# Optimization experiments

Hardware: AMD Instinct MI355X
Metric: run time of the kernel (lower is better)

Reference implementation:

```python
import jax, jax.numpy as jnp
import numpy as np


def window_partition(x, w):
    # x: [B,H,W,C] -> [B*(H/w)*(W/w), w, w, C]
    B, H, W, C = x.shape
    x = x.reshape(B, H // w, w, W // w, w, C)
    return jnp.transpose(x, (0, 1, 3, 2, 4, 5)).reshape(-1, w, w, C)


def window_reverse(xw, w, H, W):
    B = xw.shape[0] // ((H // w) * (W // w))
    x = xw.reshape(B, H // w, W // w, w, w, -1)
    return jnp.transpose(x, (0, 1, 3, 2, 4, 5)).reshape(B, H, W, -1)


def chess_partition(x, w):
    # x: [B,H,W,C] -> [B*w*w, H/w, W/w, C] (strided / chessboard grouping)
    B, H, W, C = x.shape
    x = x.reshape(B, H // w, w, W // w, w, C)
    return jnp.transpose(x, (0, 2, 4, 1, 3, 5)).reshape(-1, H // w, W // w, C)


def chess_reverse(xw, w, H, W):
    B = xw.shape[0] // (w * w)
    x = xw.reshape(B, w, w, H // w, W // w, -1)
    return jnp.transpose(x, (0, 3, 1, 4, 2, 5)).reshape(B, H, W, -1)


def _attn_block(x, wq, bq, wk, bk, wv, bv, gamma, win, part, rev):
    # x: [B,C,H,W]; 1x1-conv QKV inside partitioned windows, bmm softmax attention
    B, C, H, W = x.shape
    xw = part(jnp.transpose(x, (0, 2, 3, 1)), win)      # [B_, h, w, C]
    B_, h, w, _ = xw.shape
    xw = jnp.transpose(xw, (0, 3, 1, 2))                # [B_, C, h, w]
    q = (jnp.einsum('oc,bchw->bhwo', wq, xw) + bq).reshape(B_, h * w, -1)   # [B_,N,C/4]
    k = (jnp.einsum('oc,bchw->bohw', wk, xw) + bk[:, None, None]).reshape(B_, -1, h * w)  # [B_,C/4,N]
    v = (jnp.einsum('oc,bchw->bohw', wv, xw) + bv[:, None, None]).reshape(B_, C, h * w)   # [B_,C,N]
    attn = jax.nn.softmax(jnp.einsum('bnc,bcm->bnm', q, k), axis=-1)        # [B_,N,N]
    out = jnp.einsum('bcm,bnm->bnc', v, attn).reshape(B_, h, w, C)
    out = jnp.transpose(rev(out, win, H, W), (0, 3, 1, 2))                  # [B,C,H,W]
    return gamma * out + x


def setup_inputs() -> dict:
    key = jax.random.key(0)
    ks = jax.random.split(key, 16)
    B, C, H, W = 8, 64, 192, 192
    Cq = C // 4
    s = 0.05
    inp = {'x': jax.random.normal(ks[0], (B, C, H, W), jnp.float32)}
    names = ['wq1', 'bq1', 'wk1', 'bk1', 'wv1', 'bv1',
             'wq2', 'bq2', 'wk2', 'bk2', 'wv2', 'bv2']
    shapes = [(Cq, C), (Cq,), (Cq, C), (Cq,), (C, C), (C,),
              (Cq, C), (Cq,), (Cq, C), (Cq,), (C, C), (C,)]
    for i, (n, sh) in enumerate(zip(names, shapes)):
        inp[n] = jax.random.normal(ks[i + 1], sh, jnp.float32) * s
    # gamma is zero-init in torch; use small random so attention path contributes
    inp['gamma1'] = jax.random.normal(ks[13], (1,), jnp.float32) * 0.5
    inp['gamma2'] = jax.random.normal(ks[14], (1,), jnp.float32) * 0.5
    return inp


def reference(x, wq1, bq1, wk1, bk1, wv1, bv1, gamma1,
              wq2, bq2, wk2, bk2, wv2, bv2, gamma2):
    out1 = _attn_block(x, wq1, bq1, wk1, bk1, wv1, bv1, gamma1,
                       4, window_partition, window_reverse)
    out = _attn_block(out1, wq2, bq2, wk2, bk2, wv2, bv2, gamma2,
                      8, chess_partition, chess_reverse)
    return out
```

## Files before the change

### kernel.cpp

```cpp
#include <hip/hip_runtime.h>
#include <hip/hip_bf16.h>

#define HW 36864

typedef __attribute__((ext_vector_type(8))) short short8;
typedef __attribute__((ext_vector_type(16))) float f32x16;

__device__ __forceinline__ float BLO(unsigned u) { return __uint_as_float(u << 16); }
__device__ __forceinline__ float BHI(unsigned u) { return __uint_as_float(u & 0xffff0000u); }
__device__ __forceinline__ unsigned short f2bf(float f) {
    unsigned u = __float_as_uint(f);
    u += 0x7fffu + ((u >> 16) & 1u);
    return (unsigned short)(u >> 16);
}
__device__ __forceinline__ unsigned pk2(float lo, float hi) {
    unsigned r;
    asm("v_cvt_pk_bf16_f32 %0, %1, %2" : "=v"(r) : "v"(lo), "v"(hi));
    return r;
}
__device__ __forceinline__ void plswap(unsigned &a, unsigned &b) {
    asm volatile("v_permlane32_swap_b32 %0, %1" : "+v"(a), "+v"(b));
}

union FragW { unsigned u[4]; short8 s; };


__global__ __launch_bounds__(256) void to_nhwc_kernel(
    const float* __restrict__ x, char* __restrict__ xh)
{
    __shared__ unsigned lds[32 * 193];
    const int bid = blockIdx.x;
    const int b = bid / 192, y = bid % 192;
    const int tid = threadIdx.x;
    const int cp = tid >> 3, xq8 = tid & 7;

    const float4* rA = (const float4*)(x + ((size_t)b * 64 + 2 * cp) * HW + (size_t)y * 192);
    const float4* rB = (const float4*)(x + ((size_t)b * 64 + 2 * cp + 1) * HW + (size_t)y * 192);
    #pragma unroll
    for (int i = 0; i < 6; ++i) {
        const int f = 8 * i + xq8;
        const float4 a = rA[f];
        const float4 c = rB[f];
        const int px = f * 4;
        lds[cp * 193 + px + 0] = pk2(a.x, c.x);
        lds[cp * 193 + px + 1] = pk2(a.y, c.y);
        lds[cp * 193 + px + 2] = pk2(a.z, c.z);
        lds[cp * 193 + px + 3] = pk2(a.w, c.w);
    }
    __syncthreads();

    char* dst = xh + ((size_t)b * HW + (size_t)y * 192) * 128;
    #pragma unroll
    for (int j = 0; j < 6; ++j) {
        const int idx = j * 256 + tid;
        const int px = idx >> 3, q = idx & 7;
        uint4 v;
        v.x = lds[(4 * q + 0) * 193 + px];
        v.y = lds[(4 * q + 1) * 193 + px];
        v.z = lds[(4 * q + 2) * 193 + px];
        v.w = lds[(4 * q + 3) * 193 + px];
        *(uint4*)(dst + px * 128 + q * 16) = v;
    }
}

__global__ __launch_bounds__(256) void attn1n_kernel(
    char* __restrict__ xh,
    const float* __restrict__ wq, const float* __restrict__ bq,
    const float* __restrict__ wk, const float* __restrict__ bk,
    const float* __restrict__ wv, const float* __restrict__ bv,
    const float* __restrict__ gamma)
{
    __shared__ char smem[4 * 8192];

    const int tid   = threadIdx.x;
    const int wv_id = tid >> 6;
    const int lane  = tid & 63;
    const int l32   = lane & 31;
    const int h     = lane >> 5;
    char* VsW = smem + wv_id * 8192;

    const int gw0 = blockIdx.x * 16 + wv_id * 4;

    f32x16 zf;
    #pragma unroll
    for (int r = 0; r < 16; ++r) zf[r] = 0.f;

    FragW wqkf[4], wvf[2][4];
    {
        const float4* wrow4 = (const float4*)((l32 < 16) ? (wq + l32 * 64)
                                                         : (wk + (l32 - 16) * 64));
        #pragma unroll
        for (int cc = 0; cc < 4; ++cc) {
            const float4 a = wrow4[cc * 4 + 2 * h];
            const float4 b = wrow4[cc * 4 + 2 * h + 1];
            wqkf[cc].u[0] = pk2(a.x, a.y); wqkf[cc].u[1] = pk2(a.z, a.w);
            wqkf[cc].u[2] = pk2(b.x, b.y); wqkf[cc].u[3] = pk2(b.z, b.w);
        }
        #pragma unroll
        for (int ot = 0; ot < 2; ++ot) {
            const float4* wvr4 = (const float4*)(wv + (size_t)(ot * 32 + l32) * 64);
            #pragma unroll
            for (int cc = 0; cc < 4; ++cc) {
                const float4 a = wvr4[cc * 4 + 2 * h];
                const float4 b = wvr4[cc * 4 + 2 * h + 1];
                wvf[ot][cc].u[0] = pk2(a.x, a.y); wvf[ot][cc].u[1] = pk2(a.z, a.w);
                wvf[ot][cc].u[2] = pk2(b.x, b.y); wvf[ot][cc].u[3] = pk2(b.z, b.w);
            }
        }
    }
    float bqv[8], bkv[8], bvv[2][16];
    #pragma unroll
    for (int r = 0; r < 8; ++r) {
        const int c = (r & 3) + 8 * (r >> 2) + 4 * h;
        bqv[r] = bq[c];
        bkv[r] = bk[c];
    }
    #pragma unroll
    for (int ot = 0; ot < 2; ++ot)
        #pragma unroll
        for (int r = 0; r < 16; ++r)
            bvv[ot][r] = bv[ot * 32 + (r & 3) + 8 * (r >> 2) + 4 * h];

    FragW Ilo, Ihi;
    #pragma unroll
    for (int j = 0; j < 4; ++j) {
        const int k0 = 8 * h + 2 * j;
        unsigned lo  = (l32 == k0)      ? 0x3F80u : 0u;
        unsigned hi  = (l32 == k0 + 1)  ? 0x3F80u : 0u;
        Ilo.u[j] = lo | (hi << 16);
        unsigned lo2 = (l32 == 16 + k0)     ? 0x3F80u : 0u;
        unsigned hi2 = (l32 == 16 + k0 + 1) ? 0x3F80u : 0u;
        Ihi.u[j] = lo2 | (hi2 << 16);
    }

    size_t px1[2];
    #pragma unroll
    for (int t = 0; t < 2; ++t) {
        const int gwin = gw0 + 2 * t + (l32 >> 4);
        const int b = gwin / 2304;
        const int rem = gwin % 2304;
        const int Y = rem / 48, X = rem % 48;
        const int yy = Y * 4 + ((l32 >> 2) & 3);
        const int xx = X * 4 + (l32 & 3);
        px1[t] = ((size_t)b * HW + (size_t)yy * 192 + xx) * 128;
    }

    FragW qf[2], kf[2];
    #pragma unroll
    for (int t = 0; t < 2; ++t) {
        const char* rec = xh + px1[t];
        FragW xw[4];
        #pragma unroll
        for (int cc = 0; cc < 4; ++cc)
            xw[cc].s = *(const short8*)(rec + cc * 32 + 16 * h);

        f32x16 dqk = zf;
        #pragma unroll
        for (int cc = 0; cc < 4; ++cc)
            dqk = __builtin_amdgcn_mfma_f32_32x32x16_bf16(wqkf[cc].s, xw[cc].s, dqk, 0, 0, 0);

        {
            float q0[8];
            #pragma unroll
            for (int r = 0; r < 8; ++r) q0[r] = dqk[r] + bqv[r];
            unsigned A0 = pk2(q0[0], q0[1]), B0 = pk2(q0[2], q0[3]);
            unsigned C0 = pk2(q0[4], q0[5]), D0 = pk2(q0[6], q0[7]);
            plswap(A0, C0); plswap(B0, D0);
            qf[t].u[0] = A0; qf[t].u[1] = B0; qf[t].u[2] = C0; qf[t].u[3] = D0;
        }
        {
            float k0[8];
            #pragma unroll
            for (int r = 0; r < 8; ++r) k0[r] = dqk[8 + r] + bkv[r];
            unsigned A0 = pk2(k0[0], k0[1]), B0 = pk2(k0[2], k0[3]);
            unsigned C0 = pk2(k0[4], k0[5]), D0 = pk2(k0[6], k0[7]);
            plswap(A0, C0); plswap(B0, D0);
            kf[t].u[0] = A0; kf[t].u[1] = B0; kf[t].u[2] = C0; kf[t].u[3] = D0;
        }

        #pragma unroll
        for (int ot = 0; ot < 2; ++ot) {
            f32x16 dv = zf;
            #pragma unroll
            for (int cc = 0; cc < 4; ++cc)
                dv = __builtin_amdgcn_mfma_f32_32x32x16_bf16(wvf[ot][cc].s, xw[cc].s, dv, 0, 0, 0);
            #pragma unroll
            for (int r = 0; r < 16; ++r) {
                const int ch = ot * 32 + (r & 3) + 8 * (r >> 2) + 4 * h;
                *(unsigned short*)(VsW + ((ch * 128 + 2 * (t * 32 + l32)) ^ ((ch & 7) << 4)))
                    = f2bf(dv[r] + bvv[ot][r]);
            }
        }
    }
    __syncthreads();

    const float g = gamma[0];
    const bool wa = (l32 < 16);

    #pragma unroll
    for (int t = 0; t < 2; ++t) {
        f32x16 sT = __builtin_amdgcn_mfma_f32_32x32x16_bf16(kf[t].s, qf[t].s, zf, 0, 0, 0);

        float e[8];
        #pragma unroll
        for (int j = 0; j < 8; ++j) e[j] = __expf(wa ? sT[j] : sT[8 + j]);
        float ls = ((e[0] + e[1]) + (e[2] + e[3])) + ((e[4] + e[5]) + (e[6] + e[7]));
        ls += __shfl_xor(ls, 32);

        unsigned A0 = pk2(e[0], e[1]), B0 = pk2(e[2], e[3]);
        unsigned C0 = pk2(e[4], e[5]), D0 = pk2(e[6], e[7]);
        plswap(A0, C0); plswap(B0, D0);
        FragW pa, pb;
        pa.u[0] = wa ? A0 : 0u; pa.u[1] = wa ? B0 : 0u;
        pa.u[2] = wa ? C0 : 0u; pa.u[3] = wa ? D0 : 0u;
        pb.u[0] = wa ? 0u : A0; pb.u[1] = wa ? 0u : B0;
        pb.u[2] = wa ? 0u : C0; pb.u[3] = wa ? 0u : D0;

        f32x16 acc0 = zf, acc1 = zf;
        #pragma unroll
        for (int wsx = 0; wsx < 2; ++wsx) {
            const short8 pfrag = wsx ? pb.s : pa.s;
            const int mbase = t * 64 + wsx * 32 + 16 * h;
            const int ch0 = l32, ch1 = 32 + l32;
            const short8 v0 = *(const short8*)(VsW + ((ch0 * 128 + mbase) ^ ((ch0 & 7) << 4)));
            const short8 v1 = *(const short8*)(VsW + ((ch1 * 128 + mbase) ^ ((ch1 & 7) << 4)));
            acc0 = __builtin_amdgcn_mfma_f32_32x32x16_bf16(v0, pfrag, acc0, 0, 0, 0);
            acc1 = __builtin_amdgcn_mfma_f32_32x32x16_bf16(v1, pfrag, acc1, 0, 0, 0);
        }

        const float inv = 1.f / ls;

        char* rec = xh + px1[t];
        FragW x0, x1, x2, x3;
        x0.s = *(const short8*)(rec + 0 * 32 + 16 * h);
        x1.s = *(const short8*)(rec + 1 * 32 + 16 * h);
        x2.s = *(const short8*)(rec + 2 * 32 + 16 * h);
        x3.s = *(const short8*)(rec + 3 * 32 + 16 * h);
        f32x16 r01 = __builtin_amdgcn_mfma_f32_32x32x16_bf16(Ihi.s, x1.s, zf, 0, 0, 0);
        r01 = __builtin_amdgcn_mfma_f32_32x32x16_bf16(Ilo.s, x0.s, r01, 0, 0, 0);
        f32x16 r23 = __builtin_amdgcn_mfma_f32_32x32x16_bf16(Ihi.s, x3.s, zf, 0, 0, 0);
        r23 = __builtin_amdgcn_mfma_f32_32x32x16_bf16(Ilo.s, x2.s, r23, 0, 0, 0);

        #pragma unroll
        for (int q = 0; q < 4; ++q) {
            const float a0 = fmaf(g, acc0[4*q+0] * inv, r01[4*q+0]);
            const float a1 = fmaf(g, acc0[4*q+1] * inv, r01[4*q+1]);
            const float a2 = fmaf(g, acc0[4*q+2] * inv, r01[4*q+2]);
            const float a3 = fmaf(g, acc0[4*q+3] * inv, r01[4*q+3]);
            uint2 wA; wA.x = pk2(a0, a1); wA.y = pk2(a2, a3);
            *(uint2*)(rec + 16 * q + 8 * h) = wA;
            const float b0 = fmaf(g, acc1[4*q+0] * inv, r23[4*q+0]);
            const float b1 = fmaf(g, acc1[4*q+1] * inv, r23[4*q+1]);
            const float b2 = fmaf(g, acc1[4*q+2] * inv, r23[4*q+2]);
            const float b3 = fmaf(g, acc1[4*q+3] * inv, r23[4*q+3]);
            uint2 wB; wB.x = pk2(b0, b1); wB.y = pk2(b2, b3);
            *(uint2*)(rec + 64 + 16 * q + 8 * h) = wB;
        }
    }
}

#define KT_OFF 0
#define VS_OFF 18432

__global__ __launch_bounds__(576) void attn2n_kernel(
    char* __restrict__ xh,
    const float* __restrict__ wq, const float* __restrict__ bq,
    const float* __restrict__ wk, const float* __restrict__ bk,
    const float* __restrict__ wv, const float* __restrict__ bv,
    const float* __restrict__ gamma)
{
    __shared__ char smem[92160];

    const int wid = blockIdx.x;
    const int b  = wid >> 6;
    const int a  = wid & 7;
    const int c0 = (wid >> 3) & 7;

    const int tid = threadIdx.x;
    const int wv_id = tid >> 6;
    const int l32 = tid & 31;
    const int h   = (tid >> 5) & 1;
    const int n0  = wv_id * 64;

    f32x16 zf;
    #pragma unroll
    for (int r = 0; r < 16; ++r) zf[r] = 0.f;

    FragW wqkf[4], wvf[2][4];
    {
        const float4* wrow4 = (const float4*)((l32 < 16) ? (wq + l32 * 64)
                                                         : (wk + (l32 - 16) * 64));
        #pragma unroll
        for (int cc = 0; cc < 4; ++cc) {
            const float4 a4 = wrow4[cc * 4 + 2 * h];
            const float4 b4 = wrow4[cc * 4 + 2 * h + 1];
            wqkf[cc].u[0] = pk2(a4.x, a4.y); wqkf[cc].u[1] = pk2(a4.z, a4.w);
            wqkf[cc].u[2] = pk2(b4.x, b4.y); wqkf[cc].u[3] = pk2(b4.z, b4.w);
        }
        #pragma unroll
        for (int ot = 0; ot < 2; ++ot) {
            const float4* wvr4 = (const float4*)(wv + (size_t)(ot * 32 + l32) * 64);
            #pragma unroll
            for (int cc = 0; cc < 4; ++cc) {
                const float4 a4 = wvr4[cc * 4 + 2 * h];
                const float4 b4 = wvr4[cc * 4 + 2 * h + 1];
                wvf[ot][cc].u[0] = pk2(a4.x, a4.y); wvf[ot][cc].u[1] = pk2(a4.z, a4.w);
                wvf[ot][cc].u[2] = pk2(b4.x, b4.y); wvf[ot][cc].u[3] = pk2(b4.z, b4.w);
            }
        }
    }
    float bias_qk[16], bvv[2][16];
    #pragma unroll
    for (int r = 0; r < 8; ++r) {
        const int c = (r & 3) + 8 * (r >> 2) + 4 * h;
        bias_qk[r] = bq[c];
        bias_qk[8 + r] = bk[c];
    }
    #pragma unroll
    for (int ot = 0; ot < 2; ++ot)
        #pragma unroll
        for (int r = 0; r < 16; ++r)
            bvv[ot][r] = bv[ot * 32 + (r & 3) + 8 * (r >> 2) + 4 * h];

    FragW Ilo, Ihi;
    #pragma unroll
    for (int j = 0; j < 4; ++j) {
        const int k0 = 8 * h + 2 * j;
        unsigned lo  = (l32 == k0)      ? 0x3F80u : 0u;
        unsigned hi  = (l32 == k0 + 1)  ? 0x3F80u : 0u;
        Ilo.u[j] = lo | (hi << 16);
        unsigned lo2 = (l32 == 16 + k0)     ? 0x3F80u : 0u;
        unsigned hi2 = (l32 == 16 + k0 + 1) ? 0x3F80u : 0u;
        Ihi.u[j] = lo2 | (hi2 << 16);
    }

    size_t prec[2];
    FragW qfr[2];
    #pragma unroll
    for (int t = 0; t < 2; ++t) {
        const int m = n0 + t * 32 + l32;
        const int i = m / 24, j = m - i * 24;
        prec[t] = ((size_t)b * HW + (size_t)(a + 8 * i) * 192 + (c0 + 8 * j)) * 128;
        const char* rec = xh + prec[t];

        FragW xw[4];
        #pragma unroll
        for (int cc = 0; cc < 4; ++cc)
            xw[cc].s = *(const short8*)(rec + cc * 32 + 16 * h);

        f32x16 dqk = zf;
        #pragma unroll
        for (int cc = 0; cc < 4; ++cc)
            dqk = __builtin_amdgcn_mfma_f32_32x32x16_bf16(wqkf[cc].s, xw[cc].s, dqk, 0, 0, 0);

        {
            float q0[8];
            #pragma unroll
            for (int r = 0; r < 8; ++r) q0[r] = dqk[r] + bias_qk[r];
            unsigned A0 = pk2(q0[0], q0[1]), B0 = pk2(q0[2], q0[3]);
            unsigned C0 = pk2(q0[4], q0[5]), D0 = pk2(q0[6], q0[7]);
            plswap(A0, C0); plswap(B0, D0);
            qfr[t].u[0] = A0; qfr[t].u[1] = B0; qfr[t].u[2] = C0; qfr[t].u[3] = D0;
        }
        #pragma unroll
        for (int r = 8; r < 16; ++r) {
            const int c = (r & 3) + 8 * ((r >> 2) & 1) + 4 * h;
            *(unsigned short*)(smem + KT_OFF + ((m * 32 + 2 * c) ^ (((m >> 2) & 3) << 4)))
                = f2bf(dqk[r] + bias_qk[r]);
        }
        #pragma unroll
        for (int ot = 0; ot < 2; ++ot) {
            f32x16 dv = zf;
            #pragma unroll
            for (int cc = 0; cc < 4; ++cc)
                dv = __builtin_amdgcn_mfma_f32_32x32x16_bf16(wvf[ot][cc].s, xw[cc].s, dv, 0, 0, 0);
            #pragma unroll
            for (int r = 0; r < 16; ++r) {
                const int ch = ot * 32 + (r & 3) + 8 * (r >> 2) + 4 * h;
                *(unsigned short*)(smem + VS_OFF + ((ch * 1152 + 2 * m) ^ ((ch & 7) << 4)))
                    = f2bf(dv[r] + bvv[ot][r]);
            }
        }
    }
    __syncthreads();

    const short8 qf0 = qfr[0].s, qf1 = qfr[1].s;
    f32x16 accA = zf, accB = zf, accC = zf, accD = zf;
    float ls0 = 0.f, ls1 = 0.f;
    const int chA = l32, chB = 32 + l32;
    const int swzA = (chA & 7) << 4, swzB = (chB & 7) << 4;

    #pragma unroll 1
    for (int mt = 0; mt < 18; ++mt) {
        const int m0 = mt * 32;
        const int mr = m0 + l32;
        const short8 kf = *(const short8*)(smem + KT_OFF + ((mr * 32 + 16 * h) ^ (((mr >> 2) & 3) << 4)));
        f32x16 s0 = __builtin_amdgcn_mfma_f32_32x32x16_bf16(kf, qf0, zf, 0, 0, 0);
        f32x16 s1 = __builtin_amdgcn_mfma_f32_32x32x16_bf16(kf, qf1, zf, 0, 0, 0);

        const short8 vA0 = *(const short8*)(smem + VS_OFF + ((chA * 1152 + 2 * (m0 + 8 * h)) ^ swzA));
        const short8 vA1 = *(const short8*)(smem + VS_OFF + ((chA * 1152 + 2 * (m0 + 16 + 8 * h)) ^ swzA));
        const short8 vB0 = *(const short8*)(smem + VS_OFF + ((chB * 1152 + 2 * (m0 + 8 * h)) ^ swzB));
        const short8 vB1 = *(const short8*)(smem + VS_OFF + ((chB * 1152 + 2 * (m0 + 16 + 8 * h)) ^ swzB));

        #pragma unroll
        for (int r = 0; r < 16; ++r) s0[r] = __expf(s0[r]);
        #pragma unroll
        for (int r = 0; r < 16; ++r) s1[r] = __expf(s1[r]);
        ls0 += ((s0[0]+s0[1])+(s0[2]+s0[3])) + ((s0[4]+s0[5])+(s0[6]+s0[7]))
             + ((s0[8]+s0[9])+(s0[10]+s0[11])) + ((s0[12]+s0[13])+(s0[14]+s0[15]));
        ls1 += ((s1[0]+s1[1])+(s1[2]+s1[3])) + ((s1[4]+s1[5])+(s1[6]+s1[7]))
             + ((s1[8]+s1[9])+(s1[10]+s1[11])) + ((s1[12]+s1[13])+(s1[14]+s1[15]));

        FragW pf00, pf01, pf10, pf11;
        {
            unsigned A0 = pk2(s0[0], s0[1]), B0 = pk2(s0[2], s0[3]);
            unsigned C0 = pk2(s0[4], s0[5]), D0 = pk2(s0[6], s0[7]);
            plswap(A0, C0); plswap(B0, D0);
            pf00.u[0] = A0; pf00.u[1] = B0; pf00.u[2] = C0; pf00.u[3] = D0;
            unsigned E0 = pk2(s0[8], s0[9]),  F0 = pk2(s0[10], s0[11]);
            unsigned G0 = pk2(s0[12], s0[13]), H0 = pk2(s0[14], s0[15]);
            plswap(E0, G0); plswap(F0, H0);
            pf01.u[0] = E0; pf01.u[1] = F0; pf01.u[2] = G0; pf01.u[3] = H0;
            unsigned A1 = pk2(s1[0], s1[1]), B1 = pk2(s1[2], s1[3]);
            unsigned C1 = pk2(s1[4], s1[5]), D1 = pk2(s1[6], s1[7]);
            plswap(A1, C1); plswap(B1, D1);
            pf10.u[0] = A1; pf10.u[1] = B1; pf10.u[2] = C1; pf10.u[3] = D1;
            unsigned E1 = pk2(s1[8], s1[9]),  F1 = pk2(s1[10], s1[11]);
            unsigned G1 = pk2(s1[12], s1[13]), H1 = pk2(s1[14], s1[15]);
            plswap(E1, G1); plswap(F1, H1);
            pf11.u[0] = E1; pf11.u[1] = F1; pf11.u[2] = G1; pf11.u[3] = H1;
        }

        accA = __builtin_amdgcn_mfma_f32_32x32x16_bf16(vA0, pf00.s, accA, 0, 0, 0);
        accA = __builtin_amdgcn_mfma_f32_32x32x16_bf16(vA1, pf01.s, accA, 0, 0, 0);
        accB = __builtin_amdgcn_mfma_f32_32x32x16_bf16(vB0, pf00.s, accB, 0, 0, 0);
        accB = __builtin_amdgcn_mfma_f32_32x32x16_bf16(vB1, pf01.s, accB, 0, 0, 0);
        accC = __builtin_amdgcn_mfma_f32_32x32x16_bf16(vA0, pf10.s, accC, 0, 0, 0);
        accC = __builtin_amdgcn_mfma_f32_32x32x16_bf16(vA1, pf11.s, accC, 0, 0, 0);
        accD = __builtin_amdgcn_mfma_f32_32x32x16_bf16(vB0, pf10.s, accD, 0, 0, 0);
        accD = __builtin_amdgcn_mfma_f32_32x32x16_bf16(vB1, pf11.s, accD, 0, 0, 0);
    }

    ls0 += __shfl_xor(ls0, 32);
    ls1 += __shfl_xor(ls1, 32);
    const float g2 = gamma[0];
    const float inv0 = 1.f / ls0, inv1 = 1.f / ls1;

    #pragma unroll
    for (int t = 0; t < 2; ++t) {
        char* rec = xh + prec[t];
        FragW x0, x1, x2, x3;
        x0.s = *(const short8*)(rec + 0 * 32 + 16 * h);
        x1.s = *(const short8*)(rec + 1 * 32 + 16 * h);
        x2.s = *(const short8*)(rec + 2 * 32 + 16 * h);
        x3.s = *(const short8*)(rec + 3 * 32 + 16 * h);
        f32x16 r01 = __builtin_amdgcn_mfma_f32_32x32x16_bf16(Ihi.s, x1.s, zf, 0, 0, 0);
        r01 = __builtin_amdgcn_mfma_f32_32x32x16_bf16(Ilo.s, x0.s, r01, 0, 0, 0);
        f32x16 r23 = __builtin_amdgcn_mfma_f32_32x32x16_bf16(Ihi.s, x3.s, zf, 0, 0, 0);
        r23 = __builtin_amdgcn_mfma_f32_32x32x16_bf16(Ilo.s, x2.s, r23, 0, 0, 0);

        const f32x16 aclo = t ? accC : accA;
        const f32x16 achi = t ? accD : accB;
        const float inv = t ? inv1 : inv0;

        #pragma unroll
        for (int q = 0; q < 4; ++q) {
            const float a0 = fmaf(g2, aclo[4*q+0] * inv, r01[4*q+0]);
            const float a1 = fmaf(g2, aclo[4*q+1] * inv, r01[4*q+1]);
            const float a2 = fmaf(g2, aclo[4*q+2] * inv, r01[4*q+2]);
            const float a3 = fmaf(g2, aclo[4*q+3] * inv, r01[4*q+3]);
            uint2 wA; wA.x = pk2(a0, a1); wA.y = pk2(a2, a3);
            *(uint2*)(rec + 16 * q + 8 * h) = wA;
            const float b0 = fmaf(g2, achi[4*q+0] * inv, r23[4*q+0]);
            const float b1 = fmaf(g2, achi[4*q+1] * inv, r23[4*q+1]);
            const float b2 = fmaf(g2, achi[4*q+2] * inv, r23[4*q+2]);
            const float b3 = fmaf(g2, achi[4*q+3] * inv, r23[4*q+3]);
            uint2 wB; wB.x = pk2(b0, b1); wB.y = pk2(b2, b3);
            *(uint2*)(rec + 64 + 16 * q + 8 * h) = wB;
        }
    }
}

__global__ __launch_bounds__(256) void to_nchw_kernel(
    float* __restrict__ out, const char* __restrict__ xh)
{
    __shared__ char smem[24576];

    const int bid = blockIdx.x;
    const int b = bid / 192, y = bid % 192;
    const int tid = threadIdx.x;

    const char* src = xh + ((size_t)b * HW + (size_t)y * 192) * 128;
    #pragma unroll
    for (int k = 0; k < 6; ++k) {
        const int off = k * 4096 + tid * 16;
        const int xq = off >> 7;
        const int gq = (off >> 4) & 7;
        const short8 v = *(const short8*)(src + off);
        *(short8*)(smem + (xq << 7) + (((gq ^ (xq & 7)) << 4))) = v;
    }
    __syncthreads();

    const int w = tid >> 6, lane = tid & 63;
    const size_t rowbase = (size_t)b * 64 * HW + (size_t)y * 192;

    #pragma unroll
    for (int it = 0; it < 24; ++it) {
        const int tt = it * 4 + w;
        const int chp = tt & 31;
        const int xb = tt >> 5;
        const int xx = xb * 64 + lane;
        const int byte_in_rec = chp * 4;
        const int gq = byte_in_rec >> 4;
        const unsigned v = *(const unsigned*)(smem + (xx << 7)
                            + ((gq ^ (xx & 7)) << 4) + (byte_in_rec & 15));
        const size_t o0 = rowbase + (size_t)(2 * chp) * HW + xx;
        out[o0]      = BLO(v);
        out[o0 + HW] = BHI(v);
    }
}

extern "C" void kernel_launch(void* const* d_in, const int* in_sizes, int n_in,
                              void* d_out, int out_size, void* d_ws, size_t ws_size,
                              hipStream_t stream)
{
    const float* x   = (const float*)d_in[0];
    const float* wq1 = (const float*)d_in[1];
    const float* bq1 = (const float*)d_in[2];
    const float* wk1 = (const float*)d_in[3];
    const float* bk1 = (const float*)d_in[4];
    const float* wv1 = (const float*)d_in[5];
    const float* bv1 = (const float*)d_in[6];
    const float* wq2 = (const float*)d_in[7];
    const float* bq2 = (const float*)d_in[8];
    const float* wk2 = (const float*)d_in[9];
    const float* bk2 = (const float*)d_in[10];
    const float* wv2 = (const float*)d_in[11];
    const float* bv2 = (const float*)d_in[12];
    const float* g1  = (const float*)d_in[13];
    const float* g2  = (const float*)d_in[14];
    float* out = (float*)d_out;
    char* xh = (char*)d_ws;

    to_nhwc_kernel<<<dim3(1536), dim3(256), 0, stream>>>(x, xh);

    attn1n_kernel<<<dim3(1152), dim3(256), 0, stream>>>(
        xh, wq1, bq1, wk1, bk1, wv1, bv1, g1);

    attn2n_kernel<<<dim3(512), dim3(576), 0, stream>>>(
        xh, wq2, bq2, wk2, bk2, wv2, bv2, g2);

    to_nchw_kernel<<<dim3(1536), dim3(256), 0, stream>>>(out, xh);
}
```

Baseline: 149.9 us.

## Use exp2 with log2e-scaled Q, prefetch K, compute row sums via MFMA

Folds log2(e) into Q when it is produced, so the softmax can call exp2f instead of __expf. The chess-block loop now prefetches the next K fragment from LDS one iteration ahead. It also replaces the scalar VALU row-sum reductions and the cross-lane shuffle with MFMAs against an all-ones bf16 matrix. This moves adds from the VALU to the matrix core, but it adds four MFMAs per iteration, more accumulator registers, and sums bf16-rounded probabilities, which costs some precision.

Measured after the change: 172.6 us. +15.1%, slower.

```diff
diff --git a/kernel.cpp b/kernel.cpp
--- a/kernel.cpp
+++ b/kernel.cpp
@@ -2,6 +2,7 @@
 #include <hip/hip_bf16.h>
 
 #define HW 36864
+#define LOG2E 1.44269504088896f
 
 typedef __attribute__((ext_vector_type(8))) short short8;
 typedef __attribute__((ext_vector_type(16))) float f32x16;
@@ -162,7 +163,7 @@
         {
             float q0[8];
             #pragma unroll
-            for (int r = 0; r < 8; ++r) q0[r] = dqk[r] + bqv[r];
+            for (int r = 0; r < 8; ++r) q0[r] = (dqk[r] + bqv[r]) * LOG2E;
             unsigned A0 = pk2(q0[0], q0[1]), B0 = pk2(q0[2], q0[3]);
             unsigned C0 = pk2(q0[4], q0[5]), D0 = pk2(q0[6], q0[7]);
             plswap(A0, C0); plswap(B0, D0);
@@ -203,7 +204,7 @@
 
         float e[8];
         #pragma unroll
-        for (int j = 0; j < 8; ++j) e[j] = __expf(wa ? sT[j] : sT[8 + j]);
+        for (int j = 0; j < 8; ++j) e[j] = exp2f(wa ? sT[j] : sT[8 + j]);
         float ls = ((e[0] + e[1]) + (e[2] + e[3])) + ((e[4] + e[5]) + (e[6] + e[7]));
         ls += __shfl_xor(ls, 32);
 
@@ -333,6 +334,8 @@
         unsigned hi2 = (l32 == 16 + k0 + 1) ? 0x3F80u : 0u;
         Ihi.u[j] = lo2 | (hi2 << 16);
     }
+    FragW ones;
+    ones.u[0] = ones.u[1] = ones.u[2] = ones.u[3] = 0x3F803F80u;
 
     size_t prec[2];
     FragW qfr[2];
@@ -356,7 +359,7 @@
         {
             float q0[8];
             #pragma unroll
-            for (int r = 0; r < 8; ++r) q0[r] = dqk[r] + bias_qk[r];
+            for (int r = 0; r < 8; ++r) q0[r] = (dqk[r] + bias_qk[r]) * LOG2E;
             unsigned A0 = pk2(q0[0], q0[1]), B0 = pk2(q0[2], q0[3]);
             unsigned C0 = pk2(q0[4], q0[5]), D0 = pk2(q0[6], q0[7]);
             plswap(A0, C0); plswap(B0, D0);
@@ -386,17 +389,24 @@
 
     const short8 qf0 = qfr[0].s, qf1 = qfr[1].s;
     f32x16 accA = zf, accB = zf, accC = zf, accD = zf;
-    float ls0 = 0.f, ls1 = 0.f;
+    f32x16 accS0 = zf, accS1 = zf;
     const int chA = l32, chB = 32 + l32;
     const int swzA = (chA & 7) << 4, swzB = (chB & 7) << 4;
+
+    short8 kfc = *(const short8*)(smem + KT_OFF + ((l32 * 32 + 16 * h) ^ (((l32 >> 2) & 3) << 4)));
 
     #pragma unroll 1
     for (int mt = 0; mt < 18; ++mt) {
         const int m0 = mt * 32;
-        const int mr = m0 + l32;
-        const short8 kf = *(const short8*)(smem + KT_OFF + ((mr * 32 + 16 * h) ^ (((mr >> 2) & 3) << 4)));
-        f32x16 s0 = __builtin_amdgcn_mfma_f32_32x32x16_bf16(kf, qf0, zf, 0, 0, 0);
-        f32x16 s1 = __builtin_amdgcn_mfma_f32_32x32x16_bf16(kf, qf1, zf, 0, 0, 0);
+
+        short8 kfn = kfc;
+        if (mt < 17) {
+            const int mr = m0 + 32 + l32;
+            kfn = *(const short8*)(smem + KT_OFF + ((mr * 32 + 16 * h) ^ (((mr >> 2) & 3) << 4)));
+        }
+
+        f32x16 s0 = __builtin_amdgcn_mfma_f32_32x32x16_bf16(kfc, qf0, zf, 0, 0, 0);
+        f32x16 s1 = __builtin_amdgcn_mfma_f32_32x32x16_bf16(kfc, qf1, zf, 0, 0, 0);
 
         const short8 vA0 = *(const short8*)(smem + VS_OFF + ((chA * 1152 + 2 * (m0 + 8 * h)) ^ swzA));
         const short8 vA1 = *(const short8*)(smem + VS_OFF + ((chA * 1152 + 2 * (m0 + 16 + 8 * h)) ^ swzA));
@@ -404,13 +414,9 @@
         const short8 vB1 = *(const short8*)(smem + VS_OFF + ((chB * 1152 + 2 * (m0 + 16 + 8 * h)) ^ swzB));
 
         #pragma unroll
-        for (int r = 0; r < 16; ++r) s0[r] = __expf(s0[r]);
-        #pragma unroll
-        for (int r = 0; r < 16; ++r) s1[r] = __expf(s1[r]);
-        ls0 += ((s0[0]+s0[1])+(s0[2]+s0[3])) + ((s0[4]+s0[5])+(s0[6]+s0[7]))
-             + ((s0[8]+s0[9])+(s0[10]+s0[11])) + ((s0[12]+s0[13])+(s0[14]+s0[15]));
-        ls1 += ((s1[0]+s1[1])+(s1[2]+s1[3])) + ((s1[4]+s1[5])+(s1[6]+s1[7]))
-             + ((s1[8]+s1[9])+(s1[10]+s1[11])) + ((s1[12]+s1[13])+(s1[14]+s1[15]));
+        for (int r = 0; r < 16; ++r) s0[r] = exp2f(s0[r]);
+        #pragma unroll
+        for (int r = 0; r < 16; ++r) s1[r] = exp2f(s1[r]);
 
         FragW pf00, pf01, pf10, pf11;
         {
@@ -440,12 +446,17 @@
         accC = __builtin_amdgcn_mfma_f32_32x32x16_bf16(vA1, pf11.s, accC, 0, 0, 0);
         accD = __builtin_amdgcn_mfma_f32_32x32x16_bf16(vB0, pf10.s, accD, 0, 0, 0);
         accD = __builtin_amdgcn_mfma_f32_32x32x16_bf16(vB1, pf11.s, accD, 0, 0, 0);
-    }
-
-    ls0 += __shfl_xor(ls0, 32);
-    ls1 += __shfl_xor(ls1, 32);
+
+        accS0 = __builtin_amdgcn_mfma_f32_32x32x16_bf16(ones.s, pf00.s, accS0, 0, 0, 0);
+        accS0 = __builtin_amdgcn_mfma_f32_32x32x16_bf16(ones.s, pf01.s, accS0, 0, 0, 0);
+        accS1 = __builtin_amdgcn_mfma_f32_32x32x16_bf16(ones.s, pf10.s, accS1, 0, 0, 0);
+        accS1 = __builtin_amdgcn_mfma_f32_32x32x16_bf16(ones.s, pf11.s, accS1, 0, 0, 0);
+
+        kfc = kfn;
+    }
+
     const float g2 = gamma[0];
-    const float inv0 = 1.f / ls0, inv1 = 1.f / ls1;
+    const float inv0 = 1.f / accS0[0], inv1 = 1.f / accS1[0];
 
     #pragma unroll
     for (int t = 0; t < 2; ++t) {
```
